# Optimization experiments

Measured on AMD Instinct MI355X. Metric: run time of the kernel, lower is better.

The kernel has to match this reference:

```python
import jax, jax.numpy as jnp
import numpy as np

N = 50000      # atoms
E = 800000     # edges (flat neighbor list)
ELEM = 64      # elem_fea_len
NBR = 64       # nbr_fea_len
EPS = 1e-5


def _bn(x, gamma, beta):
    # BatchNorm1d in training mode: biased batch stats over dim 0
    mean = jnp.mean(x, axis=0)
    var = jnp.mean(jnp.square(x - mean), axis=0)
    return (x - mean) * jax.lax.rsqrt(var + EPS) * gamma + beta


def setup_inputs() -> dict:
    key = jax.random.key(0)
    ks = jax.random.split(key, 8)
    atom_in_fea = jax.random.normal(ks[0], (N, ELEM), dtype=jnp.float32)
    nbr_fea = jax.random.normal(ks[1], (E, NBR), dtype=jnp.float32)
    self_fea_idx = jnp.sort(jax.random.randint(ks[2], (E,), 0, N))
    nbr_fea_idx = jax.random.randint(ks[3], (E,), 0, N)
    d_in = 2 * ELEM + NBR
    d_out = 2 * ELEM
    W = jax.random.normal(ks[4], (d_in, d_out), dtype=jnp.float32) / np.sqrt(d_in)
    b = jax.random.normal(ks[5], (d_out,), dtype=jnp.float32) * 0.01
    bn1_gamma = jnp.ones((d_out,), jnp.float32)
    bn1_beta = jnp.zeros((d_out,), jnp.float32)
    bn2_gamma = jnp.ones((ELEM,), jnp.float32)
    bn2_beta = jnp.zeros((ELEM,), jnp.float32)
    return {
        "atom_in_fea": atom_in_fea, "nbr_fea": nbr_fea,
        "self_fea_idx": self_fea_idx, "nbr_fea_idx": nbr_fea_idx,
        "W": W, "b": b,
        "bn1_gamma": bn1_gamma, "bn1_beta": bn1_beta,
        "bn2_gamma": bn2_gamma, "bn2_beta": bn2_beta,
    }


def reference(atom_in_fea, nbr_fea, self_fea_idx, nbr_fea_idx,
              W, b, bn1_gamma, bn1_beta, bn2_gamma, bn2_beta):
    n_atoms = atom_in_fea.shape[0]
    # gather endpoint features: (E, ELEM) each
    atom_self = atom_in_fea[self_fea_idx]
    atom_nbr = atom_in_fea[nbr_fea_idx]
    total = jnp.concatenate([atom_self, atom_nbr, nbr_fea], axis=1)  # (E, 2*ELEM+NBR)
    total = total @ W + b                                            # (E, 2*ELEM)
    total = _bn(total, bn1_gamma, bn1_beta)
    filter_fea, core_fea = jnp.split(total, 2, axis=1)
    nbr_msg = jax.nn.sigmoid(filter_fea) * jax.nn.softplus(core_fea)  # (E, ELEM)
    nbr_sumed = jax.ops.segment_sum(nbr_msg, self_fea_idx, num_segments=n_atoms)
    nbr_sumed = _bn(nbr_sumed, bn2_gamma, bn2_beta)
    return jax.nn.softplus(atom_in_fea + nbr_sumed)
```

## Files before the change

### kernel.cpp

```cpp
#include <hip/hip_runtime.h>

typedef unsigned short ushort_t;
typedef __attribute__((ext_vector_type(8))) short short8;
typedef __attribute__((ext_vector_type(4))) float f32x4;

constexpr int N_ATOMS = 50000;
constexpr int N_EDGES = 800000;
constexpr int ELEM    = 64;
constexpr int D_IN    = 192;
constexpr int D_OUT   = 128;
constexpr float EPS   = 1e-5f;

constexpr int TILE_M = 64;

constexpr size_t OFF_T    = 0;
constexpr size_t OFF_NS   = OFF_T    + (size_t)N_EDGES * D_OUT * 2;
constexpr size_t OFF_ABF  = OFF_NS   + (size_t)N_ATOMS * ELEM * 4;
constexpr size_t OFF_WT   = OFF_ABF  + (size_t)N_ATOMS * ELEM * 2;
constexpr size_t OFF_BN1  = OFF_WT   + (size_t)D_OUT * D_IN * 2;
constexpr size_t OFF_SC1  = OFF_BN1  + 8 * 256 * 4;
constexpr size_t OFF_BN2  = OFF_SC1  + 256 * 4;
constexpr size_t OFF_SC2  = OFF_BN2  + 8 * 128 * 4;
constexpr size_t OFF_RS   = OFF_SC2  + 128 * 4;
constexpr size_t OFF_RE   = OFF_RS   + (size_t)N_ATOMS * 4;

__device__ __forceinline__ ushort_t f32_to_bf16(float f) {
    unsigned int u = __float_as_uint(f);
    u = (u + 0x7fffu + ((u >> 16) & 1u)) >> 16;
    return (ushort_t)u;
}
__device__ __forceinline__ float bf16_to_f32(ushort_t h) {
    return __uint_as_float(((unsigned int)h) << 16);
}
__device__ __forceinline__ float softplus_f(float x) {
    return fmaxf(x, 0.f) + __logf(1.f + __expf(-fabsf(x)));
}

__global__ void init_kernel(int* __restrict__ rs, int* __restrict__ re,
                            float* __restrict__ bn1r, float* __restrict__ bn2r) {
    int i = blockIdx.x * blockDim.x + threadIdx.x;
    if (i < N_ATOMS) { rs[i] = N_EDGES; re[i] = 0; }
    if (i < 8 * 256) bn1r[i] = 0.f;
    if (i < 8 * 128) bn2r[i] = 0.f;
}

__global__ void prep_kernel(const float* __restrict__ atom, const float* __restrict__ W,
                            ushort_t* __restrict__ atom_bf, ushort_t* __restrict__ Wt) {
    int i = blockIdx.x * blockDim.x + threadIdx.x;
    if (i < N_ATOMS * ELEM) atom_bf[i] = f32_to_bf16(atom[i]);
    if (i < D_IN * D_OUT) {
        int n = i & 127, k = i >> 7;
        Wt[n * D_IN + k] = f32_to_bf16(W[k * D_OUT + n]);
    }
}

__global__ void bounds_kernel(const int* __restrict__ sidx,
                              int* __restrict__ rs, int* __restrict__ re) {
    int e = blockIdx.x * blockDim.x + threadIdx.x;
    if (e < N_EDGES) {
        int s = sidx[e];
        if (e == 0 || sidx[e - 1] != s) rs[s] = e;
        if (e == N_EDGES - 1 || sidx[e + 1] != s) re[s] = e + 1;
    }
}

__global__ __launch_bounds__(256) void gemm_kernel(
    const ushort_t* __restrict__ atom_bf, const float* __restrict__ nbrf,
    const int* __restrict__ sidx, const int* __restrict__ nidx,
    const ushort_t* __restrict__ Wt, const float* __restrict__ bias,
    ushort_t* __restrict__ T, float* __restrict__ bn1r)
{
    __shared__ char smem[76800];
    ushort_t (*As)[200] = (ushort_t(*)[200])smem;
    ushort_t (*Bs)[200] = (ushort_t(*)[200])(smem + 25600);
    float    (*Cs)[132] = (float(*)[132])smem;

    const int tid = threadIdx.x;
    const int e0  = blockIdx.x * TILE_M;

    {
        const uint4* src = (const uint4*)Wt;
        #pragma unroll
        for (int i = 0; i < 12; ++i) {
            int c = tid + 256 * i;
            int n = c / 24, o = c % 24;
            *(uint4*)&Bs[n][o * 8] = src[c];
        }
    }
    #pragma unroll
    for (int ch = 0; ch < 2; ++ch) {
        const int* __restrict__ idx = ch ? nidx : sidx;
        #pragma unroll
        for (int i = 0; i < 2; ++i) {
            int r = (tid >> 3) + 32 * i;
            int h = tid & 7;
            const uint4* src = (const uint4*)(atom_bf + (size_t)idx[e0 + r] * 64);
            *(uint4*)&As[r][ch * 64 + h * 8] = src[h];
        }
    }
    #pragma unroll
    for (int i = 0; i < 4; ++i) {
        int r  = (tid >> 4) + 16 * i;
        int c4 = tid & 15;
        float4 v = *(const float4*)(nbrf + (size_t)(e0 + r) * 64 + c4 * 4);
        ushort4 pk;
        pk.x = f32_to_bf16(v.x); pk.y = f32_to_bf16(v.y);
        pk.z = f32_to_bf16(v.z); pk.w = f32_to_bf16(v.w);
        *(ushort4*)&As[r][128 + c4 * 4] = pk;
    }
    __syncthreads();

    const int wave = tid >> 6;
    const int lane = tid & 63;
    const int m16  = lane & 15;
    const int quad = lane >> 4;

    f32x4 acc[4][2];
    #pragma unroll
    for (int mt = 0; mt < 4; ++mt)
        #pragma unroll
        for (int nt = 0; nt < 2; ++nt)
            acc[mt][nt] = (f32x4){0.f, 0.f, 0.f, 0.f};

    #pragma unroll
    for (int ks = 0; ks < 6; ++ks) {
        int ko = ks * 32 + quad * 8;
        short8 b0 = *(const short8*)&Bs[wave * 32 + m16][ko];
        short8 b1 = *(const short8*)&Bs[wave * 32 + 16 + m16][ko];
        #pragma unroll
        for (int mt = 0; mt < 4; ++mt) {
            short8 a = *(const short8*)&As[mt * 16 + m16][ko];
            acc[mt][0] = __builtin_amdgcn_mfma_f32_16x16x32_bf16(a, b0, acc[mt][0], 0, 0, 0);
            acc[mt][1] = __builtin_amdgcn_mfma_f32_16x16x32_bf16(a, b1, acc[mt][1], 0, 0, 0);
        }
    }
    __syncthreads();

    float bias0 = bias[wave * 32 + m16];
    float bias1 = bias[wave * 32 + 16 + m16];
    #pragma unroll
    for (int mt = 0; mt < 4; ++mt) {
        int row = mt * 16 + quad * 4;
        #pragma unroll
        for (int r = 0; r < 4; ++r) {
            Cs[row + r][wave * 32 + m16]      = acc[mt][0][r] + bias0;
            Cs[row + r][wave * 32 + 16 + m16] = acc[mt][1][r] + bias1;
        }
    }
    __syncthreads();

    #pragma unroll
    for (int i = 0; i < 4; ++i) {
        int r  = (tid >> 4) + 16 * i;
        int c8 = tid & 15;
        float4 v0 = *(const float4*)&Cs[r][c8 * 8];
        float4 v1 = *(const float4*)&Cs[r][c8 * 8 + 4];
        uint4 u;
        u.x = (unsigned)f32_to_bf16(v0.x) | ((unsigned)f32_to_bf16(v0.y) << 16);
        u.y = (unsigned)f32_to_bf16(v0.z) | ((unsigned)f32_to_bf16(v0.w) << 16);
        u.z = (unsigned)f32_to_bf16(v1.x) | ((unsigned)f32_to_bf16(v1.y) << 16);
        u.w = (unsigned)f32_to_bf16(v1.z) | ((unsigned)f32_to_bf16(v1.w) << 16);
        *(uint4*)&T[(size_t)(e0 + r) * 128 + c8 * 8] = u;
    }

    {
        int c = tid & 127;
        int h = tid >> 7;
        float s = 0.f, q = 0.f;
        #pragma unroll
        for (int j = 0; j < 32; ++j) {
            float v = Cs[h * 32 + j][c];
            s += v; q += v * v;
        }
        float* rep = bn1r + (size_t)(blockIdx.x & 7) * 256;
        atomicAdd(&rep[c], s);
        atomicAdd(&rep[128 + c], q);
    }
}

__global__ void bn1_finalize(const float* __restrict__ bn1r,
                             const float* __restrict__ g1, const float* __restrict__ b1,
                             float* __restrict__ sc) {
    int c = threadIdx.x;
    float s = 0.f, q = 0.f;
    #pragma unroll
    for (int r = 0; r < 8; ++r) { s += bn1r[r * 256 + c]; q += bn1r[r * 256 + 128 + c]; }
    float mean = s * (1.f / N_EDGES);
    float var  = q * (1.f / N_EDGES) - mean * mean;
    float scale = g1[c] * rsqrtf(var + EPS);
    sc[c] = scale;
    sc[128 + c] = b1[c] - mean * scale;
}

__global__ __launch_bounds__(256) void msg_kernel(
    const ushort_t* __restrict__ T, const float* __restrict__ sc,
    const int* __restrict__ rs, const int* __restrict__ re,
    float* __restrict__ ns)
{
    int a = blockIdx.x * 4 + (threadIdx.x >> 6);
    int c = threadIdx.x & 63;
    float scf = sc[c],      shf = sc[128 + c];
    float scc = sc[64 + c], shc = sc[192 + c];
    float acc = 0.f;
    int e = rs[a], e1 = re[a];
    for (; e + 2 <= e1; e += 2) {
        const ushort_t* p0 = T + (size_t)e * 128;
        ushort_t tf0 = p0[c], tc0 = p0[64 + c];
        ushort_t tf1 = p0[128 + c], tc1 = p0[192 + c];
        float yf0 = fmaf(bf16_to_f32(tf0), scf, shf);
        float yc0 = fmaf(bf16_to_f32(tc0), scc, shc);
        float yf1 = fmaf(bf16_to_f32(tf1), scf, shf);
        float yc1 = fmaf(bf16_to_f32(tc1), scc, shc);
        acc += softplus_f(yc0) / (1.f + __expf(-yf0));
        acc += softplus_f(yc1) / (1.f + __expf(-yf1));
    }
    if (e < e1) {
        const ushort_t* p0 = T + (size_t)e * 128;
        float yf = fmaf(bf16_to_f32(p0[c]), scf, shf);
        float yc = fmaf(bf16_to_f32(p0[64 + c]), scc, shc);
        acc += softplus_f(yc) / (1.f + __expf(-yf));
    }
    ns[a * ELEM + c] = acc;
}

__global__ __launch_bounds__(256) void bn2_stats_kernel(
    const float* __restrict__ ns, float* __restrict__ bn2r)
{
    int c = threadIdx.x & 63;
    float s = 0.f, q = 0.f;
    for (int a = blockIdx.x * 4 + (threadIdx.x >> 6); a < N_ATOMS; a += 4096) {
        float v = ns[a * ELEM + c];
        s += v; q += v * v;
    }
    float* rep = bn2r + (size_t)(blockIdx.x & 7) * 128;
    atomicAdd(&rep[c], s);
    atomicAdd(&rep[64 + c], q);
}

__global__ void bn2_finalize(const float* __restrict__ bn2r,
                             const float* __restrict__ g2, const float* __restrict__ b2,
                             float* __restrict__ sc2) {
    int c = threadIdx.x;
    float s = 0.f, q = 0.f;
    #pragma unroll
    for (int r = 0; r < 8; ++r) { s += bn2r[r * 128 + c]; q += bn2r[r * 128 + 64 + c]; }
    float mean = s * (1.f / N_ATOMS);
    float var  = q * (1.f / N_ATOMS) - mean * mean;
    float scale = g2[c] * rsqrtf(var + EPS);
    sc2[c] = scale;
    sc2[64 + c] = b2[c] - mean * scale;
}

__global__ void final_kernel(const float* __restrict__ atom, const float* __restrict__ ns,
                             const float* __restrict__ sc2, float* __restrict__ out)
{
    int i = blockIdx.x * blockDim.x + threadIdx.x;
    if (i < N_ATOMS * ELEM) {
        int c = i & 63;
        float x = atom[i] + fmaf(ns[i], sc2[c], sc2[64 + c]);
        out[i] = softplus_f(x);
    }
}

extern "C" void kernel_launch(void* const* d_in, const int* in_sizes, int n_in,
                              void* d_out, int out_size, void* d_ws, size_t ws_size,
                              hipStream_t stream) {
    const float* atom = (const float*)d_in[0];
    const float* nbrf = (const float*)d_in[1];
    const int*   sidx = (const int*)d_in[2];
    const int*   nidx = (const int*)d_in[3];
    const float* W    = (const float*)d_in[4];
    const float* bias = (const float*)d_in[5];
    const float* g1   = (const float*)d_in[6];
    const float* b1   = (const float*)d_in[7];
    const float* g2   = (const float*)d_in[8];
    const float* b2   = (const float*)d_in[9];
    float* out = (float*)d_out;
    char*  ws  = (char*)d_ws;

    ushort_t* T    = (ushort_t*)(ws + OFF_T);
    float* ns      = (float*)(ws + OFF_NS);
    ushort_t* abf  = (ushort_t*)(ws + OFF_ABF);
    ushort_t* Wt   = (ushort_t*)(ws + OFF_WT);
    float* bn1r    = (float*)(ws + OFF_BN1);
    float* sc1     = (float*)(ws + OFF_SC1);
    float* bn2r    = (float*)(ws + OFF_BN2);
    float* sc2     = (float*)(ws + OFF_SC2);
    int*   rs      = (int*)(ws + OFF_RS);
    int*   re      = (int*)(ws + OFF_RE);

    hipLaunchKernelGGL(init_kernel, dim3((N_ATOMS + 255) / 256), dim3(256), 0, stream,
                       rs, re, bn1r, bn2r);
    hipLaunchKernelGGL(prep_kernel, dim3((N_ATOMS * ELEM + 255) / 256), dim3(256), 0, stream,
                       atom, W, abf, Wt);
    hipLaunchKernelGGL(bounds_kernel, dim3((N_EDGES + 255) / 256), dim3(256), 0, stream,
                       sidx, rs, re);
    hipLaunchKernelGGL(gemm_kernel, dim3(N_EDGES / TILE_M), dim3(256), 0, stream,
                       abf, nbrf, sidx, nidx, Wt, bias, T, bn1r);
    hipLaunchKernelGGL(bn1_finalize, dim3(1), dim3(128), 0, stream, bn1r, g1, b1, sc1);
    hipLaunchKernelGGL(msg_kernel, dim3(N_ATOMS / 4), dim3(256), 0, stream,
                       T, sc1, rs, re, ns);
    hipLaunchKernelGGL(bn2_stats_kernel, dim3(1024), dim3(256), 0, stream, ns, bn2r);
    hipLaunchKernelGGL(bn2_finalize, dim3(1), dim3(64), 0, stream, bn2r, g2, b2, sc2);
    hipLaunchKernelGGL(final_kernel, dim3((N_ATOMS * ELEM + 255) / 256), dim3(256), 0, stream,
                       atom, ns, sc2, out);
}
```

Before: 469.8 us.

## Recompute edge GEMM in message kernel instead of materializing bf16 T buffer

Splits the edge GEMM into a stats-only pass that computes BN1 sums from register accumulators, and a second pass that recomputes the GEMM and fuses BN1, the gating activation and a segmented atomic scatter into the atom sums. This drops the write and re-read of the 800k x 128 bf16 intermediate and the CSR bounds kernels. In exchange the gathers, the nbr_fea read and the MFMA work are done twice, and the per-atom reduction now uses global float atomics, which makes the sums order-nondeterministic. It also merges the init and prep kernels, loads W fragments directly into registers, and doubles the BN stat replicas.

```diff
diff --git a/kernel.cpp b/kernel.cpp
--- a/kernel.cpp
+++ b/kernel.cpp
@@ -12,17 +12,15 @@
 constexpr float EPS   = 1e-5f;
 
 constexpr int TILE_M = 64;
-
-constexpr size_t OFF_T    = 0;
-constexpr size_t OFF_NS   = OFF_T    + (size_t)N_EDGES * D_OUT * 2;
+constexpr int NREP   = 16;
+
+constexpr size_t OFF_NS   = 0;
 constexpr size_t OFF_ABF  = OFF_NS   + (size_t)N_ATOMS * ELEM * 4;
 constexpr size_t OFF_WT   = OFF_ABF  + (size_t)N_ATOMS * ELEM * 2;
 constexpr size_t OFF_BN1  = OFF_WT   + (size_t)D_OUT * D_IN * 2;
-constexpr size_t OFF_SC1  = OFF_BN1  + 8 * 256 * 4;
+constexpr size_t OFF_SC1  = OFF_BN1  + NREP * 256 * 4;
 constexpr size_t OFF_BN2  = OFF_SC1  + 256 * 4;
-constexpr size_t OFF_SC2  = OFF_BN2  + 8 * 128 * 4;
-constexpr size_t OFF_RS   = OFF_SC2  + 128 * 4;
-constexpr size_t OFF_RE   = OFF_RS   + (size_t)N_ATOMS * 4;
+constexpr size_t OFF_SC2  = OFF_BN2  + NREP * 128 * 4;
 
 __device__ __forceinline__ ushort_t f32_to_bf16(float f) {
     unsigned int u = __float_as_uint(f);
@@ -36,57 +34,26 @@
     return fmaxf(x, 0.f) + __logf(1.f + __expf(-fabsf(x)));
 }
 
-__global__ void init_kernel(int* __restrict__ rs, int* __restrict__ re,
-                            float* __restrict__ bn1r, float* __restrict__ bn2r) {
+__global__ void prep_init_kernel(const float* __restrict__ atom, const float* __restrict__ W,
+                                 ushort_t* __restrict__ abf, ushort_t* __restrict__ Wt,
+                                 float* __restrict__ ns,
+                                 float* __restrict__ bn1r, float* __restrict__ bn2r) {
     int i = blockIdx.x * blockDim.x + threadIdx.x;
-    if (i < N_ATOMS) { rs[i] = N_EDGES; re[i] = 0; }
-    if (i < 8 * 256) bn1r[i] = 0.f;
-    if (i < 8 * 128) bn2r[i] = 0.f;
-}
-
-__global__ void prep_kernel(const float* __restrict__ atom, const float* __restrict__ W,
-                            ushort_t* __restrict__ atom_bf, ushort_t* __restrict__ Wt) {
-    int i = blockIdx.x * blockDim.x + threadIdx.x;
-    if (i < N_ATOMS * ELEM) atom_bf[i] = f32_to_bf16(atom[i]);
+    if (i < N_ATOMS * ELEM) { abf[i] = f32_to_bf16(atom[i]); ns[i] = 0.f; }
     if (i < D_IN * D_OUT) {
-        int n = i & 127, k = i >> 7;
-        Wt[n * D_IN + k] = f32_to_bf16(W[k * D_OUT + n]);
-    }
-}
-
-__global__ void bounds_kernel(const int* __restrict__ sidx,
-                              int* __restrict__ rs, int* __restrict__ re) {
-    int e = blockIdx.x * blockDim.x + threadIdx.x;
-    if (e < N_EDGES) {
-        int s = sidx[e];
-        if (e == 0 || sidx[e - 1] != s) rs[s] = e;
-        if (e == N_EDGES - 1 || sidx[e + 1] != s) re[s] = e + 1;
-    }
-}
-
-__global__ __launch_bounds__(256) void gemm_kernel(
-    const ushort_t* __restrict__ atom_bf, const float* __restrict__ nbrf,
-    const int* __restrict__ sidx, const int* __restrict__ nidx,
-    const ushort_t* __restrict__ Wt, const float* __restrict__ bias,
-    ushort_t* __restrict__ T, float* __restrict__ bn1r)
-{
-    __shared__ char smem[76800];
-    ushort_t (*As)[200] = (ushort_t(*)[200])smem;
-    ushort_t (*Bs)[200] = (ushort_t(*)[200])(smem + 25600);
-    float    (*Cs)[132] = (float(*)[132])smem;
-
-    const int tid = threadIdx.x;
-    const int e0  = blockIdx.x * TILE_M;
-
-    {
-        const uint4* src = (const uint4*)Wt;
-        #pragma unroll
-        for (int i = 0; i < 12; ++i) {
-            int c = tid + 256 * i;
-            int n = c / 24, o = c % 24;
-            *(uint4*)&Bs[n][o * 8] = src[c];
-        }
-    }
+        int k = i >> 7, n = i & 127;
+        Wt[n * D_IN + k] = f32_to_bf16(W[i]);
+    }
+    if (i < NREP * 256) bn1r[i] = 0.f;
+    if (i < NREP * 128) bn2r[i] = 0.f;
+}
+
+__device__ __forceinline__ void stage_A(ushort_t (*As)[200],
+                                        const ushort_t* __restrict__ abf,
+                                        const float* __restrict__ nbrf,
+                                        const int* __restrict__ sidx,
+                                        const int* __restrict__ nidx,
+                                        int e0, int tid) {
     #pragma unroll
     for (int ch = 0; ch < 2; ++ch) {
         const int* __restrict__ idx = ch ? nidx : sidx;
@@ -94,7 +61,7 @@
         for (int i = 0; i < 2; ++i) {
             int r = (tid >> 3) + 32 * i;
             int h = tid & 7;
-            const uint4* src = (const uint4*)(atom_bf + (size_t)idx[e0 + r] * 64);
+            const uint4* src = (const uint4*)(abf + (size_t)idx[e0 + r] * 64);
             *(uint4*)&As[r][ch * 64 + h * 8] = src[h];
         }
     }
@@ -108,73 +75,68 @@
         pk.z = f32_to_bf16(v.z); pk.w = f32_to_bf16(v.w);
         *(ushort4*)&As[r][128 + c4 * 4] = pk;
     }
+}
+
+__global__ __launch_bounds__(256) void stats_kernel(
+    const ushort_t* __restrict__ abf, const float* __restrict__ nbrf,
+    const int* __restrict__ sidx, const int* __restrict__ nidx,
+    const ushort_t* __restrict__ Wt, const float* __restrict__ bias,
+    float* __restrict__ bn1r)
+{
+    __shared__ __align__(16) ushort_t As[64][200];
+    const int tid = threadIdx.x;
+    const int e0  = blockIdx.x * TILE_M;
+
+    stage_A(As, abf, nbrf, sidx, nidx, e0, tid);
+
+    const int wave = tid >> 6, lane = tid & 63;
+    const int m16 = lane & 15, quad = lane >> 4;
+
+    short8 bfrag[2][6];
+    #pragma unroll
+    for (int nt = 0; nt < 2; ++nt) {
+        const ushort_t* bp = Wt + (size_t)(wave * 32 + nt * 16 + m16) * D_IN + quad * 8;
+        #pragma unroll
+        for (int ks = 0; ks < 6; ++ks) bfrag[nt][ks] = *(const short8*)(bp + ks * 32);
+    }
     __syncthreads();
 
-    const int wave = tid >> 6;
-    const int lane = tid & 63;
-    const int m16  = lane & 15;
-    const int quad = lane >> 4;
-
     f32x4 acc[4][2];
     #pragma unroll
     for (int mt = 0; mt < 4; ++mt)
         #pragma unroll
-        for (int nt = 0; nt < 2; ++nt)
-            acc[mt][nt] = (f32x4){0.f, 0.f, 0.f, 0.f};
+        for (int nt = 0; nt < 2; ++nt) acc[mt][nt] = (f32x4){0.f, 0.f, 0.f, 0.f};
 
     #pragma unroll
     for (int ks = 0; ks < 6; ++ks) {
         int ko = ks * 32 + quad * 8;
-        short8 b0 = *(const short8*)&Bs[wave * 32 + m16][ko];
-        short8 b1 = *(const short8*)&Bs[wave * 32 + 16 + m16][ko];
         #pragma unroll
         for (int mt = 0; mt < 4; ++mt) {
             short8 a = *(const short8*)&As[mt * 16 + m16][ko];
-            acc[mt][0] = __builtin_amdgcn_mfma_f32_16x16x32_bf16(a, b0, acc[mt][0], 0, 0, 0);
-            acc[mt][1] = __builtin_amdgcn_mfma_f32_16x16x32_bf16(a, b1, acc[mt][1], 0, 0, 0);
-        }
-    }
-    __syncthreads();
-
-    float bias0 = bias[wave * 32 + m16];
-    float bias1 = bias[wave * 32 + 16 + m16];
-    #pragma unroll
-    for (int mt = 0; mt < 4; ++mt) {
-        int row = mt * 16 + quad * 4;
-        #pragma unroll
-        for (int r = 0; r < 4; ++r) {
-            Cs[row + r][wave * 32 + m16]      = acc[mt][0][r] + bias0;
-            Cs[row + r][wave * 32 + 16 + m16] = acc[mt][1][r] + bias1;
-        }
-    }
-    __syncthreads();
-
-    #pragma unroll
-    for (int i = 0; i < 4; ++i) {
-        int r  = (tid >> 4) + 16 * i;
-        int c8 = tid & 15;
-        float4 v0 = *(const float4*)&Cs[r][c8 * 8];
-        float4 v1 = *(const float4*)&Cs[r][c8 * 8 + 4];
-        uint4 u;
-        u.x = (unsigned)f32_to_bf16(v0.x) | ((unsigned)f32_to_bf16(v0.y) << 16);
-        u.y = (unsigned)f32_to_bf16(v0.z) | ((unsigned)f32_to_bf16(v0.w) << 16);
-        u.z = (unsigned)f32_to_bf16(v1.x) | ((unsigned)f32_to_bf16(v1.y) << 16);
-        u.w = (unsigned)f32_to_bf16(v1.z) | ((unsigned)f32_to_bf16(v1.w) << 16);
-        *(uint4*)&T[(size_t)(e0 + r) * 128 + c8 * 8] = u;
-    }
-
-    {
-        int c = tid & 127;
-        int h = tid >> 7;
+            acc[mt][0] = __builtin_amdgcn_mfma_f32_16x16x32_bf16(a, bfrag[0][ks], acc[mt][0], 0, 0, 0);
+            acc[mt][1] = __builtin_amdgcn_mfma_f32_16x16x32_bf16(a, bfrag[1][ks], acc[mt][1], 0, 0, 0);
+        }
+    }
+
+    float* rep = bn1r + (size_t)(blockIdx.x & (NREP - 1)) * 256;
+    #pragma unroll
+    for (int nt = 0; nt < 2; ++nt) {
+        int c = wave * 32 + nt * 16 + m16;
+        float b = bias[c];
         float s = 0.f, q = 0.f;
         #pragma unroll
-        for (int j = 0; j < 32; ++j) {
-            float v = Cs[h * 32 + j][c];
-            s += v; q += v * v;
-        }
-        float* rep = bn1r + (size_t)(blockIdx.x & 7) * 256;
-        atomicAdd(&rep[c], s);
-        atomicAdd(&rep[128 + c], q);
+        for (int mt = 0; mt < 4; ++mt)
+            #pragma unroll
+            for (int r = 0; r < 4; ++r) {
+                float v = acc[mt][nt][r] + b;
+                s += v; q += v * v;
+            }
+        s += __shfl_xor(s, 16); s += __shfl_xor(s, 32);
+        q += __shfl_xor(q, 16); q += __shfl_xor(q, 32);
+        if (quad == 0) {
+            atomicAdd(&rep[c], s);
+            atomicAdd(&rep[128 + c], q);
+        }
     }
 }
 
@@ -184,7 +146,7 @@
     int c = threadIdx.x;
     float s = 0.f, q = 0.f;
     #pragma unroll
-    for (int r = 0; r < 8; ++r) { s += bn1r[r * 256 + c]; q += bn1r[r * 256 + 128 + c]; }
+    for (int r = 0; r < NREP; ++r) { s += bn1r[r * 256 + c]; q += bn1r[r * 256 + 128 + c]; }
     float mean = s * (1.f / N_EDGES);
     float var  = q * (1.f / N_EDGES) - mean * mean;
     float scale = g1[c] * rsqrtf(var + EPS);
@@ -193,34 +155,87 @@
 }
 
 __global__ __launch_bounds__(256) void msg_kernel(
-    const ushort_t* __restrict__ T, const float* __restrict__ sc,
-    const int* __restrict__ rs, const int* __restrict__ re,
-    float* __restrict__ ns)
+    const ushort_t* __restrict__ abf, const float* __restrict__ nbrf,
+    const int* __restrict__ sidx, const int* __restrict__ nidx,
+    const ushort_t* __restrict__ Wt, const float* __restrict__ bias,
+    const float* __restrict__ sc, float* __restrict__ ns)
 {
-    int a = blockIdx.x * 4 + (threadIdx.x >> 6);
-    int c = threadIdx.x & 63;
-    float scf = sc[c],      shf = sc[128 + c];
-    float scc = sc[64 + c], shc = sc[192 + c];
-    float acc = 0.f;
-    int e = rs[a], e1 = re[a];
-    for (; e + 2 <= e1; e += 2) {
-        const ushort_t* p0 = T + (size_t)e * 128;
-        ushort_t tf0 = p0[c], tc0 = p0[64 + c];
-        ushort_t tf1 = p0[128 + c], tc1 = p0[192 + c];
-        float yf0 = fmaf(bf16_to_f32(tf0), scf, shf);
-        float yc0 = fmaf(bf16_to_f32(tc0), scc, shc);
-        float yf1 = fmaf(bf16_to_f32(tf1), scf, shf);
-        float yc1 = fmaf(bf16_to_f32(tc1), scc, shc);
-        acc += softplus_f(yc0) / (1.f + __expf(-yf0));
-        acc += softplus_f(yc1) / (1.f + __expf(-yf1));
-    }
-    if (e < e1) {
-        const ushort_t* p0 = T + (size_t)e * 128;
-        float yf = fmaf(bf16_to_f32(p0[c]), scf, shf);
-        float yc = fmaf(bf16_to_f32(p0[64 + c]), scc, shc);
-        acc += softplus_f(yc) / (1.f + __expf(-yf));
-    }
-    ns[a * ELEM + c] = acc;
+    __shared__ __align__(16) char smem[25600];
+    ushort_t (*As)[200] = (ushort_t(*)[200])smem;
+    float    (*Ms)[68]  = (float(*)[68])smem;
+    __shared__ int ss[64];
+
+    const int tid = threadIdx.x;
+    const int e0  = blockIdx.x * TILE_M;
+
+    stage_A(As, abf, nbrf, sidx, nidx, e0, tid);
+    if (tid < 64) ss[tid] = sidx[e0 + tid];
+
+    const int wave = tid >> 6, lane = tid & 63;
+    const int m16 = lane & 15, quad = lane >> 4;
+    const int cf = wave * 16 + m16;
+    const int cc = 64 + cf;
+
+    short8 bfrag[2][6];
+    {
+        const ushort_t* bp0 = Wt + (size_t)cf * D_IN + quad * 8;
+        const ushort_t* bp1 = Wt + (size_t)cc * D_IN + quad * 8;
+        #pragma unroll
+        for (int ks = 0; ks < 6; ++ks) {
+            bfrag[0][ks] = *(const short8*)(bp0 + ks * 32);
+            bfrag[1][ks] = *(const short8*)(bp1 + ks * 32);
+        }
+    }
+    __syncthreads();
+
+    f32x4 acc[4][2];
+    #pragma unroll
+    for (int mt = 0; mt < 4; ++mt)
+        #pragma unroll
+        for (int nt = 0; nt < 2; ++nt) acc[mt][nt] = (f32x4){0.f, 0.f, 0.f, 0.f};
+
+    #pragma unroll
+    for (int ks = 0; ks < 6; ++ks) {
+        int ko = ks * 32 + quad * 8;
+        #pragma unroll
+        for (int mt = 0; mt < 4; ++mt) {
+            short8 a = *(const short8*)&As[mt * 16 + m16][ko];
+            acc[mt][0] = __builtin_amdgcn_mfma_f32_16x16x32_bf16(a, bfrag[0][ks], acc[mt][0], 0, 0, 0);
+            acc[mt][1] = __builtin_amdgcn_mfma_f32_16x16x32_bf16(a, bfrag[1][ks], acc[mt][1], 0, 0, 0);
+        }
+    }
+    __syncthreads();
+
+    {
+        float bf_ = bias[cf], bc_ = bias[cc];
+        float scf = sc[cf], shf = sc[128 + cf];
+        float scc = sc[cc], shc = sc[128 + cc];
+        #pragma unroll
+        for (int mt = 0; mt < 4; ++mt) {
+            int row = mt * 16 + quad * 4;
+            #pragma unroll
+            for (int r = 0; r < 4; ++r) {
+                float yf = fmaf(acc[mt][0][r] + bf_, scf, shf);
+                float yc = fmaf(acc[mt][1][r] + bc_, scc, shc);
+                Ms[row + r][cf] = softplus_f(yc) / (1.f + __expf(-yf));
+            }
+        }
+    }
+    __syncthreads();
+
+    {
+        int v = tid >> 6, c = tid & 63;
+        int base = v * 16;
+        int cur = ss[base];
+        float a = 0.f;
+        #pragma unroll
+        for (int r = 0; r < 16; ++r) {
+            int s = ss[base + r];
+            if (s != cur) { atomicAdd(&ns[(size_t)cur * 64 + c], a); cur = s; a = 0.f; }
+            a += Ms[base + r][c];
+        }
+        atomicAdd(&ns[(size_t)cur * 64 + c], a);
+    }
 }
 
 __global__ __launch_bounds__(256) void bn2_stats_kernel(
@@ -232,7 +247,7 @@
         float v = ns[a * ELEM + c];
         s += v; q += v * v;
     }
-    float* rep = bn2r + (size_t)(blockIdx.x & 7) * 128;
+    float* rep = bn2r + (size_t)(blockIdx.x & (NREP - 1)) * 128;
     atomicAdd(&rep[c], s);
     atomicAdd(&rep[64 + c], q);
 }
@@ -243,7 +258,7 @@
     int c = threadIdx.x;
     float s = 0.f, q = 0.f;
     #pragma unroll
-    for (int r = 0; r < 8; ++r) { s += bn2r[r * 128 + c]; q += bn2r[r * 128 + 64 + c]; }
+    for (int r = 0; r < NREP; ++r) { s += bn2r[r * 128 + c]; q += bn2r[r * 128 + 64 + c]; }
     float mean = s * (1.f / N_ATOMS);
     float var  = q * (1.f / N_ATOMS) - mean * mean;
     float scale = g2[c] * rsqrtf(var + EPS);
@@ -278,28 +293,21 @@
     float* out = (float*)d_out;
     char*  ws  = (char*)d_ws;
 
-    ushort_t* T    = (ushort_t*)(ws + OFF_T);
-    float* ns      = (float*)(ws + OFF_NS);
+    float*    ns   = (float*)(ws + OFF_NS);
     ushort_t* abf  = (ushort_t*)(ws + OFF_ABF);
     ushort_t* Wt   = (ushort_t*)(ws + OFF_WT);
-    float* bn1r    = (float*)(ws + OFF_BN1);
-    float* sc1     = (float*)(ws + OFF_SC1);
-    float* bn2r    = (float*)(ws + OFF_BN2);
-    float* sc2     = (float*)(ws + OFF_SC2);
-    int*   rs      = (int*)(ws + OFF_RS);
-    int*   re      = (int*)(ws + OFF_RE);
-
-    hipLaunchKernelGGL(init_kernel, dim3((N_ATOMS + 255) / 256), dim3(256), 0, stream,
-                       rs, re, bn1r, bn2r);
-    hipLaunchKernelGGL(prep_kernel, dim3((N_ATOMS * ELEM + 255) / 256), dim3(256), 0, stream,
-                       atom, W, abf, Wt);
-    hipLaunchKernelGGL(bounds_kernel, dim3((N_EDGES + 255) / 256), dim3(256), 0, stream,
-                       sidx, rs, re);
-    hipLaunchKernelGGL(gemm_kernel, dim3(N_EDGES / TILE_M), dim3(256), 0, stream,
-                       abf, nbrf, sidx, nidx, Wt, bias, T, bn1r);
+    float*    bn1r = (float*)(ws + OFF_BN1);
+    float*    sc1  = (float*)(ws + OFF_SC1);
+    float*    bn2r = (float*)(ws + OFF_BN2);
+    float*    sc2  = (float*)(ws + OFF_SC2);
+
+    hipLaunchKernelGGL(prep_init_kernel, dim3((N_ATOMS * ELEM + 255) / 256), dim3(256), 0, stream,
+                       atom, W, abf, Wt, ns, bn1r, bn2r);
+    hipLaunchKernelGGL(stats_kernel, dim3(N_EDGES / TILE_M), dim3(256), 0, stream,
+                       abf, nbrf, sidx, nidx, Wt, bias, bn1r);
     hipLaunchKernelGGL(bn1_finalize, dim3(1), dim3(128), 0, stream, bn1r, g1, b1, sc1);
-    hipLaunchKernelGGL(msg_kernel, dim3(N_ATOMS / 4), dim3(256), 0, stream,
-                       T, sc1, rs, re, ns);
+    hipLaunchKernelGGL(msg_kernel, dim3(N_EDGES / TILE_M), dim3(256), 0, stream,
+                       abf, nbrf, sidx, nidx, Wt, bias, sc1, ns);
     hipLaunchKernelGGL(bn2_stats_kernel, dim3(1024), dim3(256), 0, stream, ns, bn2r);
     hipLaunchKernelGGL(bn2_finalize, dim3(1), dim3(64), 0, stream, bn2r, g2, b2, sc2);
     hipLaunchKernelGGL(final_kernel, dim3((N_ATOMS * ELEM + 255) / 256), dim3(256), 0, stream,
```

Result: no change. 461.0 us (-1.9%).
